# Performance work log

Measured on AMD Instinct MI355X. Metric: run time of the kernel, lower is better.

## Reference

```python
import jax, jax.numpy as jnp
import numpy as np

ALPHA = 0.2  # LeakyReLU negative slope
NEG_INF = -1e12


def setup_inputs() -> dict:
    key = jax.random.key(0)
    k1, k2, k3, k4, k5 = jax.random.split(key, 5)
    N, F = 4096, 512
    inp = jax.random.normal(k1, (N, F), dtype=jnp.float32)
    adj = jax.random.randint(k2, (N, N), 0, 2).astype(jnp.float32)
    W = jax.random.normal(k3, (F, F), dtype=jnp.float32) * (1.414 / np.sqrt(F))
    a = jax.random.normal(k4, (2 * F, 1), dtype=jnp.float32) * 0.05
    wtrans = jax.random.normal(k5, (2 * F, F), dtype=jnp.float32) * (1.414 / np.sqrt(1.5 * F))
    return {"inp": inp, "adj": adj, "W": W, "a": a, "wtrans": wtrans}


def reference(inp, adj, W, a, wtrans):
    F_out = W.shape[1]
    h = inp @ W                                   # [N, F]
    Wh1 = h @ a[:F_out, :]                        # [N, 1]
    Wh2 = h @ a[F_out:, :]                        # [N, 1]
    e = jax.nn.leaky_relu(Wh1 + Wh2.T, ALPHA)     # [N, N]
    mask = adj > 0
    attention = jax.nn.softmax(jnp.where(mask, e, NEG_INF), axis=1)
    negative_attention = -jax.nn.softmax(jnp.where(mask, -e, NEG_INF), axis=1)
    # dropout p=0.0 (eval mode): identity
    h_prime = attention @ inp                     # [N, F_in]
    h_prime_negative = negative_attention @ inp   # [N, F_in]
    h_prime_double = jnp.concatenate([h_prime, h_prime_negative], axis=1)
    new_h_prime = h_prime_double @ wtrans         # [N, F_out]
    return jax.nn.elu(new_h_prime)
```

## Files before the change

kernel.cpp:

```cpp
#include <hip/hip_runtime.h>
#include <hip/hip_bf16.h>

#define N_NODES 4096
#define F_DIM   512
#define KTOT    8192
#define KSPLIT  8
#define NSTEPS  32
#define LOG2E   1.44269504f

#define SLAB_E   8192ull
#define PANEL_E  262144ull
#define ZBLK_E   4194304ull

typedef __attribute__((ext_vector_type(8))) short bf16x8;
typedef __attribute__((ext_vector_type(4))) float f32x4;

__device__ inline unsigned short f2bf(float f) {
  union { float f; unsigned u; } c; c.f = f;
  unsigned r = c.u + 0x7fffu + ((c.u >> 16) & 1u);
  return (unsigned short)(r >> 16);
}
__device__ inline float bf2f(unsigned short u) {
  union { unsigned u; float f; } c; c.u = ((unsigned)u) << 16;
  return c.f;
}

__global__ void k_compute_v(const float* __restrict__ W, const float* __restrict__ a,
                            float* __restrict__ v1, float* __restrict__ v2) {
  int r = blockIdx.x, l = threadIdx.x;
  float s1 = 0.f, s2 = 0.f;
  for (int c = l; c < F_DIM; c += 64) {
    float w = W[(size_t)r * F_DIM + c];
    s1 += w * a[c];
    s2 += w * a[F_DIM + c];
  }
#pragma unroll
  for (int off = 32; off > 0; off >>= 1) { s1 += __shfl_down(s1, off); s2 += __shfl_down(s2, off); }
  if (l == 0) { v1[r] = s1; v2[r] = s2; }
}

__global__ void k_compute_wh(const float* __restrict__ inp, const float* __restrict__ v1,
                             const float* __restrict__ v2, float* __restrict__ Wh1,
                             float* __restrict__ Wh2) {
  int i = blockIdx.x, l = threadIdx.x;
  float s1 = 0.f, s2 = 0.f;
  for (int c = l; c < F_DIM; c += 64) {
    float x = inp[(size_t)i * F_DIM + c];
    s1 += x * v1[c];
    s2 += x * v2[c];
  }
#pragma unroll
  for (int off = 32; off > 0; off >>= 1) { s1 += __shfl_down(s1, off); s2 += __shfl_down(s2, off); }
  if (l == 0) { Wh1[i] = s1 * LOG2E; Wh2[i] = s2 * LOG2E; }
}

__global__ void k_transpose_bf16(const float* __restrict__ src, unsigned short* __restrict__ dst,
                                 int R, int C) {
  __shared__ float tile[32][33];
  int c0 = blockIdx.x * 32, r0 = blockIdx.y * 32;
  int tx = threadIdx.x, ty = threadIdx.y;
#pragma unroll
  for (int i = ty; i < 32; i += 8)
    tile[i][tx] = src[(size_t)(r0 + i) * C + c0 + tx];
  __syncthreads();
#pragma unroll
  for (int i = ty; i < 32; i += 8)
    dst[(size_t)(c0 + i) * R + r0 + tx] = f2bf(tile[tx][i]);
}

__global__ __launch_bounds__(256) void k_y(const float* __restrict__ inp,
                                           const unsigned short* __restrict__ wtT,
                                           unsigned short* __restrict__ YT) {
  int tid = threadIdx.x, l = tid & 63, w = tid >> 6;
  int row = l & 15, kg = l >> 4;
  int jt = blockIdx.x * 64 + w * 16;
  int cb = blockIdx.y * 64;
  f32x4 acc1[4] = {}, acc2[4] = {};
  const float* ap = inp + (size_t)(jt + row) * F_DIM + kg * 8;
  for (int k0 = 0; k0 < F_DIM; k0 += 32) {
    float4 f0 = *(const float4*)(ap + k0);
    float4 f1 = *(const float4*)(ap + k0 + 4);
    bf16x8 a;
    a[0] = (short)f2bf(f0.x); a[1] = (short)f2bf(f0.y); a[2] = (short)f2bf(f0.z); a[3] = (short)f2bf(f0.w);
    a[4] = (short)f2bf(f1.x); a[5] = (short)f2bf(f1.y); a[6] = (short)f2bf(f1.z); a[7] = (short)f2bf(f1.w);
#pragma unroll
    for (int n = 0; n < 4; n++) {
      const unsigned short* bp = wtT + (size_t)(cb + n * 16 + row) * 1024 + kg * 8 + k0;
      bf16x8 b1 = *(const bf16x8*)(bp);
      bf16x8 b2 = *(const bf16x8*)(bp + F_DIM);
      acc1[n] = __builtin_amdgcn_mfma_f32_16x16x32_bf16(a, b1, acc1[n], 0, 0, 0);
      acc2[n] = __builtin_amdgcn_mfma_f32_16x16x32_bf16(a, b2, acc2[n], 0, 0, 0);
    }
  }
  int jb = jt + kg * 4;
#pragma unroll
  for (int n = 0; n < 4; n++) {
    int f = cb + n * 16 + row;
    ushort4 o1, o2;
    o1.x = f2bf(acc1[n][0]); o1.y = f2bf(acc1[n][1]); o1.z = f2bf(acc1[n][2]); o1.w = f2bf(acc1[n][3]);
    o2.x = f2bf(acc2[n][0]); o2.y = f2bf(acc2[n][1]); o2.z = f2bf(acc2[n][2]); o2.w = f2bf(acc2[n][3]);
    *(ushort4*)(YT + (size_t)f * KTOT + jb) = o1;
    *(ushort4*)(YT + (size_t)f * KTOT + 4096 + jb) = o2;
  }
}

__global__ __launch_bounds__(256) void k_p(const float* __restrict__ adj,
                                           const float* __restrict__ Wh1,
                                           const float* __restrict__ Wh2,
                                           unsigned short* __restrict__ Pcat) {
  int i = blockIdx.x, t = threadIdx.x;
  float w1 = Wh1[i];
  int j0 = t * 16;
  const float* ar = adj + (size_t)i * N_NODES + j0;
  float4 A0 = *(const float4*)(ar);
  float4 A1 = *(const float4*)(ar + 4);
  float4 A2 = *(const float4*)(ar + 8);
  float4 A3 = *(const float4*)(ar + 12);
  float am[16] = {A0.x, A0.y, A0.z, A0.w, A1.x, A1.y, A1.z, A1.w,
                  A2.x, A2.y, A2.z, A2.w, A3.x, A3.y, A3.z, A3.w};
  float4 wv0 = *(const float4*)(Wh2 + j0);
  float4 wv1 = *(const float4*)(Wh2 + j0 + 4);
  float4 wv2 = *(const float4*)(Wh2 + j0 + 8);
  float4 wv3 = *(const float4*)(Wh2 + j0 + 12);
  float w2[16] = {wv0.x, wv0.y, wv0.z, wv0.w, wv1.x, wv1.y, wv1.z, wv1.w,
                  wv2.x, wv2.y, wv2.z, wv2.w, wv3.x, wv3.y, wv3.z, wv3.w};
  float pe[16], ne[16];
  float sp = 0.f, sn = 0.f;
#pragma unroll
  for (int r = 0; r < 16; r++) {
    float s = w1 + w2[r];
    float e = fmaxf(s, 0.2f * s);
    float p = exp2f(e);
    float n = exp2f(-e);
    if (!(am[r] > 0.f)) { p = 0.f; n = 0.f; }
    pe[r] = p; ne[r] = n; sp += p; sn += n;
  }
#pragma unroll
  for (int off = 1; off < 64; off <<= 1) { sp += __shfl_xor(sp, off); sn += __shfl_xor(sn, off); }
  __shared__ float red[2][4];
  int wv = t >> 6, ln = t & 63;
  if (ln == 0) { red[0][wv] = sp; red[1][wv] = sn; }
  __syncthreads();
  sp = red[0][0] + red[0][1] + red[0][2] + red[0][3];
  sn = red[1][0] + red[1][1] + red[1][2] + red[1][3];
  float rp = 1.f / sp;
  float rn = -1.f / sn;

  int zz = j0 >> 10;
  int local = j0 & 1023;
  size_t base = (size_t)zz * ZBLK_E + (size_t)(i >> 8) * PANEL_E
              + (size_t)(local >> 5) * SLAB_E + (size_t)(i & 255) * 32 + (local & 31);
  bf16x8 o;
#pragma unroll
  for (int r = 0; r < 8; r++) o[r] = (short)f2bf(pe[r] * rp);
  *(bf16x8*)(Pcat + base) = o;
#pragma unroll
  for (int r = 0; r < 8; r++) o[r] = (short)f2bf(pe[8 + r] * rp);
  *(bf16x8*)(Pcat + base + 8) = o;
#pragma unroll
  for (int r = 0; r < 8; r++) o[r] = (short)f2bf(ne[r] * rn);
  *(bf16x8*)(Pcat + base + 4 * ZBLK_E) = o;
#pragma unroll
  for (int r = 0; r < 8; r++) o[r] = (short)f2bf(ne[8 + r] * rn);
  *(bf16x8*)(Pcat + base + 4 * ZBLK_E + 8) = o;
}

#define GLOAD16(gp, lp) __builtin_amdgcn_global_load_lds( \
    (const __attribute__((address_space(1))) unsigned int*)(gp), \
    (__attribute__((address_space(3))) unsigned int*)(lp), 16, 0, 0)

__global__ __launch_bounds__(512, 2) void k_pv(const unsigned short* __restrict__ Pcat,
                                               const unsigned short* __restrict__ YT,
                                               unsigned short* __restrict__ part) {
  __shared__ unsigned short Ab[3][256 * 32];
  __shared__ unsigned short Bb[3][256 * 32];
  int t = threadIdx.x;
  int l = t & 63, w = t >> 6;
  int la = l & 15, kg = l >> 4;
  int wr = w >> 2, wc = w & 3;
  int bm0 = blockIdx.x * 256, bn0 = blockIdx.y * 256;
  int z = blockIdx.z;
  size_t kbase = (size_t)z * (KTOT / KSPLIT);

  int seg = ((t & 3) ^ ((t >> 3) & 3)) << 4;
  const char* gA = (const char*)(Pcat + ((size_t)z * 16 + blockIdx.x) * PANEL_E)
                 + (t >> 2) * 64 + seg;
  const char* gB = (const char*)YT + ((size_t)(bn0 + (t >> 2)) * KTOT + kbase) * 2 + seg;
  const size_t rstepB = (size_t)128 * KTOT * 2;

  int aswz = (kg ^ ((la >> 1) & 3)) << 4;
  int abase = (wr * 128 + la) * 64 + aswz;
  int bbase = (wc * 64 + la) * 64 + aswz;

  f32x4 acc[8][4] = {};

#define STAGE3(buf, st) do { \
    const char* _ga = gA + (size_t)(st) * 16384; \
    const char* _gb = gB + (size_t)(st) * 64; \
    char* _la = (char*)&Ab[buf][0] + w * 1024; \
    char* _lb = (char*)&Bb[buf][0] + w * 1024; \
    GLOAD16(_ga, _la); \
    GLOAD16(_ga + 8192, _la + 8192); \
    GLOAD16(_gb, _lb); \
    GLOAD16(_gb + rstepB, _lb + 8192); \
  } while (0)

  STAGE3(0, 0);
  STAGE3(1, 1);
  for (int st = 0; st < NSTEPS; st++) {
    __builtin_amdgcn_s_barrier();
    int buf = st % 3;
    if (st + 2 < NSTEPS) {
      STAGE3((st + 2) % 3, st + 2);
      asm volatile("s_waitcnt vmcnt(8)" ::: "memory");
    } else if (st + 1 < NSTEPS) {
      asm volatile("s_waitcnt vmcnt(4)" ::: "memory");
    } else {
      asm volatile("s_waitcnt vmcnt(0)" ::: "memory");
    }
    __builtin_amdgcn_s_barrier();

    const char* Abp = (const char*)&Ab[buf][0];
    const char* Bbp = (const char*)&Bb[buf][0];
    bf16x8 af[8], bfr[4];
#pragma unroll
    for (int mi = 0; mi < 8; mi++) af[mi] = *(const bf16x8*)(Abp + abase + mi * 1024);
#pragma unroll
    for (int ni = 0; ni < 4; ni++) bfr[ni] = *(const bf16x8*)(Bbp + bbase + ni * 1024);
    __builtin_amdgcn_s_setprio(1);
#pragma unroll
    for (int mi = 0; mi < 8; mi++)
#pragma unroll
      for (int ni = 0; ni < 4; ni++)
        acc[mi][ni] = __builtin_amdgcn_mfma_f32_16x16x32_bf16(af[mi], bfr[ni], acc[mi][ni], 0, 0, 0);
    __builtin_amdgcn_s_setprio(0);
  }

  unsigned short* po = part + (size_t)z * (N_NODES * F_DIM);
#pragma unroll
  for (int mi = 0; mi < 8; mi++)
#pragma unroll
    for (int ni = 0; ni < 4; ni++)
#pragma unroll
      for (int q = 0; q < 4; q++) {
        int i_ = bm0 + wr * 128 + mi * 16 + kg * 4 + q;
        int f_ = bn0 + wc * 64 + ni * 16 + la;
        po[(size_t)i_ * F_DIM + f_] = f2bf(acc[mi][ni][q]);
      }
}

__global__ __launch_bounds__(256) void k_fin(const unsigned short* __restrict__ part,
                                             float* __restrict__ out) {
  size_t idx = ((size_t)blockIdx.x * 256 + threadIdx.x) * 8;
  float s[8] = {};
#pragma unroll
  for (int p = 0; p < KSPLIT; p++) {
    bf16x8 v = *(const bf16x8*)(part + (size_t)p * (N_NODES * F_DIM) + idx);
#pragma unroll
    for (int q = 0; q < 8; q++) s[q] += bf2f((unsigned short)v[q]);
  }
#pragma unroll
  for (int q = 0; q < 8; q++) s[q] = s[q] > 0.f ? s[q] : (__expf(s[q]) - 1.f);
  float4 o0 = make_float4(s[0], s[1], s[2], s[3]);
  float4 o1 = make_float4(s[4], s[5], s[6], s[7]);
  *(float4*)(out + idx) = o0;
  *(float4*)(out + idx + 4) = o1;
}

extern "C" void kernel_launch(void* const* d_in, const int* in_sizes, int n_in,
                              void* d_out, int out_size, void* d_ws, size_t ws_size,
                              hipStream_t stream) {
  (void)in_sizes; (void)n_in; (void)out_size; (void)ws_size;
  const float* inp    = (const float*)d_in[0];
  const float* adj    = (const float*)d_in[1];
  const float* W      = (const float*)d_in[2];
  const float* a      = (const float*)d_in[3];
  const float* wtrans = (const float*)d_in[4];
  float* out = (float*)d_out;

  char* ws = (char*)d_ws;
  float* v1  = (float*)ws;
  float* v2  = (float*)(ws + 2048);
  float* Wh1 = (float*)(ws + 4096);
  float* Wh2 = (float*)(ws + 20480);

  const size_t PSZ = (size_t)N_NODES * F_DIM * 2;
  char* regA = ws + 65536;
  unsigned short* wtT  = (unsigned short*)regA;
  unsigned short* part = (unsigned short*)regA;
  unsigned short* YT   = (unsigned short*)(regA + KSPLIT * PSZ);
  unsigned short* Pcat = (unsigned short*)(regA + KSPLIT * PSZ + 8388608);

  k_compute_v<<<512, 64, 0, stream>>>(W, a, v1, v2);
  k_compute_wh<<<4096, 64, 0, stream>>>(inp, v1, v2, Wh1, Wh2);
  k_transpose_bf16<<<dim3(16, 32), dim3(32, 8), 0, stream>>>(wtrans, wtT, 1024, F_DIM);
  k_y<<<dim3(64, 8), 256, 0, stream>>>(inp, wtT, YT);
  k_p<<<4096, 256, 0, stream>>>(adj, Wh1, Wh2, Pcat);
  k_pv<<<dim3(16, 2, KSPLIT), 512, 0, stream>>>(Pcat, YT, part);
  k_fin<<<1024, 256, 0, stream>>>(part, out);
}
```

Before: 132.4 us.

## Load A tiles via registers with contiguous 32-byte reads and double-buffered regs

```diff
diff --git a/kernel.cpp b/kernel.cpp
--- a/kernel.cpp
+++ b/kernel.cpp
@@ -169,7 +169,7 @@
     (const __attribute__((address_space(1))) unsigned int*)(gp), \
     (__attribute__((address_space(3))) unsigned int*)(lp), 16, 0, 0)
 
-__global__ __launch_bounds__(512, 2) void k_pv(const unsigned short* __restrict__ Pcat,
+__global__ __launch_bounds__(512, 1) void k_pv(const unsigned short* __restrict__ Pcat,
                                                const unsigned short* __restrict__ YT,
                                                unsigned short* __restrict__ part) {
   __shared__ unsigned short Ab[3][256 * 32];
@@ -182,9 +182,12 @@
   int z = blockIdx.z;
   size_t kbase = (size_t)z * (KTOT / KSPLIT);
 
+  int rr = t >> 1, hh = t & 1, xk = (rr >> 1) & 3;
+  const char* gA = (const char*)(Pcat + ((size_t)z * 16 + blockIdx.x) * PANEL_E) + t * 32;
+  int wo0 = rr * 64 + ((2 * hh) ^ xk) * 16;
+  int wo1 = rr * 64 + ((2 * hh + 1) ^ xk) * 16;
+
   int seg = ((t & 3) ^ ((t >> 3) & 3)) << 4;
-  const char* gA = (const char*)(Pcat + ((size_t)z * 16 + blockIdx.x) * PANEL_E)
-                 + (t >> 2) * 64 + seg;
   const char* gB = (const char*)YT + ((size_t)(bn0 + (t >> 2)) * KTOT + kbase) * 2 + seg;
   const size_t rstepB = (size_t)128 * KTOT * 2;
 
@@ -193,35 +196,28 @@
   int bbase = (wc * 64 + la) * 64 + aswz;
 
   f32x4 acc[8][4] = {};
-
-#define STAGE3(buf, st) do { \
-    const char* _ga = gA + (size_t)(st) * 16384; \
-    const char* _gb = gB + (size_t)(st) * 64; \
-    char* _la = (char*)&Ab[buf][0] + w * 1024; \
-    char* _lb = (char*)&Bb[buf][0] + w * 1024; \
-    GLOAD16(_ga, _la); \
-    GLOAD16(_ga + 8192, _la + 8192); \
-    GLOAD16(_gb, _lb); \
-    GLOAD16(_gb + rstepB, _lb + 8192); \
-  } while (0)
-
-  STAGE3(0, 0);
-  STAGE3(1, 1);
-  for (int st = 0; st < NSTEPS; st++) {
-    __builtin_amdgcn_s_barrier();
-    int buf = st % 3;
-    if (st + 2 < NSTEPS) {
-      STAGE3((st + 2) % 3, st + 2);
-      asm volatile("s_waitcnt vmcnt(8)" ::: "memory");
-    } else if (st + 1 < NSTEPS) {
-      asm volatile("s_waitcnt vmcnt(4)" ::: "memory");
-    } else {
-      asm volatile("s_waitcnt vmcnt(0)" ::: "memory");
-    }
-    __builtin_amdgcn_s_barrier();
-
-    const char* Abp = (const char*)&Ab[buf][0];
-    const char* Bbp = (const char*)&Bb[buf][0];
+  f32x4 aE0, aE1, aO0, aO1;
+
+  auto issueA = [&](f32x4& r0, f32x4& r1, int stq) {
+    const char* p = gA + (size_t)stq * 16384;
+    asm volatile("global_load_dwordx4 %0, %2, off\n\t"
+                 "global_load_dwordx4 %1, %2, off offset:16"
+                 : "=v"(r0), "=v"(r1) : "v"(p) : "memory");
+  };
+  auto writeA = [&](int slot, const f32x4& r0, const f32x4& r1) {
+    char* b = (char*)&Ab[slot][0];
+    *(f32x4*)(b + wo0) = r0;
+    *(f32x4*)(b + wo1) = r1;
+  };
+  auto stageB = [&](int buf, int stq) {
+    const char* p = gB + (size_t)stq * 64;
+    char* lb = (char*)&Bb[buf][0] + w * 1024;
+    GLOAD16(p, lb);
+    GLOAD16(p + rstepB, lb + 8192);
+  };
+  auto compute = [&](int slot) {
+    const char* Abp = (const char*)&Ab[slot][0];
+    const char* Bbp = (const char*)&Bb[slot][0];
     bf16x8 af[8], bfr[4];
 #pragma unroll
     for (int mi = 0; mi < 8; mi++) af[mi] = *(const bf16x8*)(Abp + abase + mi * 1024);
@@ -234,6 +230,33 @@
       for (int ni = 0; ni < 4; ni++)
         acc[mi][ni] = __builtin_amdgcn_mfma_f32_16x16x32_bf16(af[mi], bfr[ni], acc[mi][ni], 0, 0, 0);
     __builtin_amdgcn_s_setprio(0);
+  };
+  auto body = [&](int st, f32x4& w0, f32x4& w1, f32x4& i0, f32x4& i1) {
+    __builtin_amdgcn_s_barrier();
+    if (st + 2 < NSTEPS) {
+      issueA(i0, i1, st + 2);
+      stageB((st + 2) % 3, st + 2);
+    }
+    if (st + 2 < NSTEPS)      asm volatile("s_waitcnt vmcnt(6)" ::: "memory");
+    else if (st + 1 < NSTEPS) asm volatile("s_waitcnt vmcnt(2)" ::: "memory");
+    else                      asm volatile("s_waitcnt vmcnt(0)" ::: "memory");
+    if (st + 1 < NSTEPS) writeA((st + 1) % 3, w0, w1);
+    asm volatile("s_waitcnt lgkmcnt(0)" ::: "memory");
+    __builtin_amdgcn_s_barrier();
+    compute(st % 3);
+  };
+
+  issueA(aE0, aE1, 0);
+  issueA(aO0, aO1, 1);
+  stageB(0, 0);
+  stageB(1, 1);
+  asm volatile("s_waitcnt vmcnt(6)" ::: "memory");
+  writeA(0, aE0, aE1);
+  asm volatile("s_waitcnt lgkmcnt(0)" ::: "memory");
+
+  for (int st = 0; st < NSTEPS; st += 2) {
+    body(st,     aO0, aO1, aE0, aE1);
+    body(st + 1, aE0, aE1, aO0, aO1);
   }
 
   unsigned short* po = part + (size_t)z * (N_NODES * F_DIM);
```

New measurement: 132.0 us. About the same (-0.3%).

## Split prefetch and MFMA loop into interleaved A/B halves for finer overlap

Applied to the files above, without the earlier changes.

```diff
diff --git a/kernel.cpp b/kernel.cpp
--- a/kernel.cpp
+++ b/kernel.cpp
@@ -194,46 +194,60 @@
 
   f32x4 acc[8][4] = {};
 
-#define STAGE3(buf, st) do { \
+#define STAGE_A(buf, st) do { \
     const char* _ga = gA + (size_t)(st) * 16384; \
-    const char* _gb = gB + (size_t)(st) * 64; \
     char* _la = (char*)&Ab[buf][0] + w * 1024; \
-    char* _lb = (char*)&Bb[buf][0] + w * 1024; \
     GLOAD16(_ga, _la); \
     GLOAD16(_ga + 8192, _la + 8192); \
+  } while (0)
+#define STAGE_B(buf, st) do { \
+    const char* _gb = gB + (size_t)(st) * 64; \
+    char* _lb = (char*)&Bb[buf][0] + w * 1024; \
     GLOAD16(_gb, _lb); \
     GLOAD16(_gb + rstepB, _lb + 8192); \
   } while (0)
 
-  STAGE3(0, 0);
-  STAGE3(1, 1);
+  STAGE_A(0, 0); STAGE_B(0, 0);
+  STAGE_A(1, 1); STAGE_B(1, 1);
+
+  int rs = 0, rx = 2;
   for (int st = 0; st < NSTEPS; st++) {
-    __builtin_amdgcn_s_barrier();
-    int buf = st % 3;
-    if (st + 2 < NSTEPS) {
-      STAGE3((st + 2) % 3, st + 2);
-      asm volatile("s_waitcnt vmcnt(8)" ::: "memory");
-    } else if (st + 1 < NSTEPS) {
-      asm volatile("s_waitcnt vmcnt(4)" ::: "memory");
-    } else {
-      asm volatile("s_waitcnt vmcnt(0)" ::: "memory");
+    if (st + 2 < NSTEPS) STAGE_A(rx, st + 2);
+    if (st + 2 < NSTEPS)      asm volatile("s_waitcnt vmcnt(6)" ::: "memory");
+    else if (st + 1 < NSTEPS) asm volatile("s_waitcnt vmcnt(4)" ::: "memory");
+    else                      asm volatile("s_waitcnt vmcnt(0)" ::: "memory");
+    asm volatile("s_barrier" ::: "memory");
+
+    const char* Abp = (const char*)&Ab[rs][0];
+    const char* Bbp = (const char*)&Bb[rs][0];
+    bf16x8 af[8], bf0, bf1;
+#pragma unroll
+    for (int mi = 0; mi < 8; mi++) af[mi] = *(const bf16x8*)(Abp + abase + mi * 1024);
+    bf0 = *(const bf16x8*)(Bbp + bbase);
+    bf1 = *(const bf16x8*)(Bbp + bbase + 1024);
+    __builtin_amdgcn_s_setprio(1);
+#pragma unroll
+    for (int mi = 0; mi < 8; mi++) {
+      acc[mi][0] = __builtin_amdgcn_mfma_f32_16x16x32_bf16(af[mi], bf0, acc[mi][0], 0, 0, 0);
+      acc[mi][1] = __builtin_amdgcn_mfma_f32_16x16x32_bf16(af[mi], bf1, acc[mi][1], 0, 0, 0);
     }
-    __builtin_amdgcn_s_barrier();
-
-    const char* Abp = (const char*)&Ab[buf][0];
-    const char* Bbp = (const char*)&Bb[buf][0];
-    bf16x8 af[8], bfr[4];
-#pragma unroll
-    for (int mi = 0; mi < 8; mi++) af[mi] = *(const bf16x8*)(Abp + abase + mi * 1024);
-#pragma unroll
-    for (int ni = 0; ni < 4; ni++) bfr[ni] = *(const bf16x8*)(Bbp + bbase + ni * 1024);
+    __builtin_amdgcn_s_setprio(0);
+    asm volatile("s_barrier" ::: "memory");
+
+    if (st + 2 < NSTEPS) STAGE_B(rx, st + 2);
+    bf16x8 bf2 = *(const bf16x8*)(Bbp + bbase + 2048);
+    bf16x8 bf3 = *(const bf16x8*)(Bbp + bbase + 3072);
     __builtin_amdgcn_s_setprio(1);
 #pragma unroll
-    for (int mi = 0; mi < 8; mi++)
-#pragma unroll
-      for (int ni = 0; ni < 4; ni++)
-        acc[mi][ni] = __builtin_amdgcn_mfma_f32_16x16x32_bf16(af[mi], bfr[ni], acc[mi][ni], 0, 0, 0);
+    for (int mi = 0; mi < 8; mi++) {
+      acc[mi][2] = __builtin_amdgcn_mfma_f32_16x16x32_bf16(af[mi], bf2, acc[mi][2], 0, 0, 0);
+      acc[mi][3] = __builtin_amdgcn_mfma_f32_16x16x32_bf16(af[mi], bf3, acc[mi][3], 0, 0, 0);
+    }
     __builtin_amdgcn_s_setprio(0);
+    asm volatile("s_barrier" ::: "memory");
+
+    rs = (rs + 1 == 3) ? 0 : rs + 1;
+    rx = (rx + 1 == 3) ? 0 : rx + 1;
   }
 
   unsigned short* po = part + (size_t)z * (N_NODES * F_DIM);
```

Result: slower. 137.9 us (+4.2%).
